# Performance work log

Measured on AMD Instinct MI355X. Metric: run time of the kernel, lower is better.

Reference implementation:

```python
import jax, jax.numpy as jnp
import numpy as np

MAX_LENGTH = 50
EOS_TOKEN = 0
SOS_TOKEN = 1
B, H, V = 64, 1024, 32000


def setup_inputs() -> dict:
    key = jax.random.key(0)
    ks = jax.random.split(key, 11)
    xav = float(np.sqrt(6.0 / (H + H)))  # xavier_uniform over [H,H] slabs
    inv = 1.0 / float(np.sqrt(H))
    return {
        "encoder_output": jax.random.normal(ks[0], (MAX_LENGTH, B, H), jnp.float32),
        "std": jax.random.normal(ks[1], (MAX_LENGTH, B, V), jnp.float32),
        "h": jax.random.normal(ks[2], (B, H), jnp.float32),
        "c": jax.random.normal(ks[3], (B, H), jnp.float32),
        "emb": jax.random.normal(ks[4], (V, H), jnp.float32),
        "w_ih": jax.random.uniform(ks[5], (4, H, H), jnp.float32, -xav, xav),
        "w_hh": jax.random.uniform(ks[6], (4, H, H), jnp.float32, -xav, xav),
        "b_ih": jax.random.normal(ks[7], (4, H), jnp.float32),
        "b_hh": jax.random.normal(ks[8], (4, H), jnp.float32),
        "out_w": jax.random.uniform(ks[9], (H, V), jnp.float32, -inv, inv),
        "out_b": jax.random.uniform(ks[10], (V,), jnp.float32, -inv, inv),
    }


def reference(encoder_output, std, h, c, emb, w_ih, w_hh, b_ih, b_hh, out_w, out_b):
    batch = encoder_output.shape[1]
    tok0 = jnp.full((batch,), SOS_TOKEN, dtype=jnp.int64)

    def step(carry, std_t):
        h, c, tok, active = carry  # active: scalar bool, True while decoding
        x = emb[tok]  # [B,H] embedding gather
        # gates: [4,B,H] = x@W_ih + h@W_hh + biases
        g = (jnp.einsum("bh,ghk->gbk", x, w_ih) + b_ih[:, None, :]
             + jnp.einsum("bh,ghk->gbk", h, w_hh) + b_hh[:, None, :])
        ingate = jax.nn.sigmoid(g[0])
        forgetgate = jax.nn.sigmoid(g[1])
        cellgate = jnp.tanh(g[2])
        outgate = jax.nn.sigmoid(g[3])
        c_new = forgetgate * c + ingate * cellgate
        h_new = outgate * jnp.tanh(c_new)
        logits = h_new @ out_w + out_b + std_t  # [B,V]
        tok_new = jnp.argmax(logits, axis=1).astype(jnp.int64)
        # only commit the step while the decode loop is active
        h2 = jnp.where(active, h_new, h)
        c2 = jnp.where(active, c_new, c)
        tok2 = jnp.where(active, tok_new, tok)
        tok_out = jnp.where(active, tok_new, jnp.zeros_like(tok_new))
        next_active = jnp.logical_and(active, jnp.max(tok_new) > EOS_TOKEN)
        return (h2, c2, tok2, next_active), tok_out

    (h, c, _, _), output_all = jax.lax.scan(
        step, (h, c, tok0, jnp.array(True)), std)
    return output_all, h
```

## Files before the change

kernel.cpp:

```cpp
#include <hip/hip_runtime.h>
#include <cstdint>
#include <cstddef>

#define B 64
#define H 1024
#define V 32000
#define T 50
#define VT 2000
#define GNT 256
#define SW 16.0f
#define SL 2048.0f
#define INV_HI (1.0f/16.0f)
#define INV_LO (1.0f/32768.0f)

typedef _Float16 f16;
typedef _Float16 half8 __attribute__((ext_vector_type(8)));
typedef float f32x4 __attribute__((ext_vector_type(4)));

__device__ __forceinline__ float sigmoidf_(float x) { return 1.0f / (1.0f + expf(-x)); }


__global__ __launch_bounds__(256) void k_packw(const float* __restrict__ out_w,
                                               f16* __restrict__ Whi, f16* __restrict__ Wlo)
{
    const int vt = blockIdx.x >> 3, cg = blockIdx.x & 7;
    const int chunk = cg * 4 + (threadIdx.x >> 6);
    const int q = (threadIdx.x >> 4) & 3, vl = threadIdx.x & 15;
    const int lane = q * 16 + vl;
    half8 h8, l8;
    #pragma unroll
    for (int j = 0; j < 8; ++j) {
        const int k = chunk * 32 + q * 8 + j;
        const float w = out_w[(size_t)k * V + vt * 16 + vl] * SW;
        const f16 hi = (f16)w;
        h8[j] = hi;
        l8[j] = (f16)((w - (float)hi) * SL);
    }
    const size_t pos = ((size_t)(vt * 32 + chunk) * 64 + lane) * 8;
    *(half8*)&Whi[pos] = h8;
    *(half8*)&Wlo[pos] = l8;
}

__global__ __launch_bounds__(256) void k_packg(const float* __restrict__ w_ih,
                                               const float* __restrict__ w_hh,
                                               f16* __restrict__ Ghi, f16* __restrict__ Glo)
{
    const int nt = blockIdx.x >> 4, cg = blockIdx.x & 15;
    const int chunk = cg * 4 + (threadIdx.x >> 6);
    const int q = (threadIdx.x >> 4) & 3, vl = threadIdx.x & 15;
    const int lane = q * 16 + vl;
    const int kk = vl >> 2, g = vl & 3;
    const int kcol = nt * 4 + kk;
    half8 h8, l8;
    #pragma unroll
    for (int j = 0; j < 8; ++j) {
        const int K = chunk * 32 + q * 8 + j;
        const float w = ((K < 1024)
            ? w_ih[(size_t)g * H * H + (size_t)K * H + kcol]
            : w_hh[(size_t)g * H * H + (size_t)(K - 1024) * H + kcol]) * SW;
        const f16 hi = (f16)w;
        h8[j] = hi;
        l8[j] = (f16)((w - (float)hi) * SL);
    }
    const size_t pos = ((size_t)(nt * 64 + chunk) * 64 + lane) * 8;
    *(half8*)&Ghi[pos] = h8;
    *(half8*)&Glo[pos] = l8;
}

__global__ void k_packbias(const float* __restrict__ b_ih, const float* __restrict__ b_hh,
                           float* __restrict__ biasp)
{
    const int n = blockIdx.x * 256 + threadIdx.x;
    const int blk = n >> 4, rem = n & 15, kk = rem >> 2, g = rem & 3;
    const int kcol = blk * 4 + kk;
    biasp[n] = b_ih[g * H + kcol] + b_hh[g * H + kcol];
}

__global__ void k_init(const float* __restrict__ h_in, const float* __restrict__ c_in,
                       const float* __restrict__ emb,
                       float* __restrict__ h_t, float* __restrict__ c_t,
                       f16* __restrict__ Axh, f16* __restrict__ Axl,
                       f16* __restrict__ Ah0h, f16* __restrict__ Ah0l,
                       unsigned long long* __restrict__ keys, int* __restrict__ active,
                       float* __restrict__ out)
{
    if (blockIdx.x == 64) {
        for (int i = threadIdx.x; i < T * B; i += 256) out[i] = 0.0f;
        if (threadIdx.x < B) keys[threadIdx.x] = 0ull;
        if (threadIdx.x == 0) { active[0] = 1; active[1] = 0; }
        return;
    }
    const int b = blockIdx.x, mt = b >> 4;
    #pragma unroll
    for (int i = 0; i < 4; ++i) {
        const int k = threadIdx.x * 4 + i;
        const float hv = h_in[b * H + k];
        const float cv = c_in[b * H + k];
        h_t[k * B + b] = hv;
        c_t[k * B + b] = cv;
        const float xv = emb[H + k];
        const int chunk = k >> 5, lane = ((k >> 3) & 3) * 16 + (b & 15), j = k & 7;
        const size_t pos = ((size_t)(chunk * 4 + mt) * 64 + lane) * 8 + j;
        f16 hi = (f16)hv;
        Ah0h[pos] = hi; Ah0l[pos] = (f16)((hv - (float)hi) * SL);
        hi = (f16)xv;
        Axh[pos] = hi; Axl[pos] = (f16)((xv - (float)hi) * SL);
    }
}

__global__ __launch_bounds__(256) void k_gates(
    const f16* __restrict__ Ghi, const f16* __restrict__ Glo,
    const f16* __restrict__ Axh, const f16* __restrict__ Axl,
    const f16* __restrict__ Ahh, const f16* __restrict__ Ahl,
    f16* __restrict__ Anh, f16* __restrict__ Anl,
    const float* __restrict__ biasp, float* __restrict__ h_t, float* __restrict__ c_t,
    const int* __restrict__ active, int t)
{
    if (!active[t & 1]) return;
    const int tid = threadIdx.x;
    const int s = tid >> 6, lane = tid & 63;
    const int quad = lane >> 4, vl = lane & 15;
    const int nt = blockIdx.x;

    f32x4 acc0[4], acc1[4];
    #pragma unroll
    for (int mt = 0; mt < 4; ++mt) {
        acc0[mt] = (f32x4){0.f, 0.f, 0.f, 0.f};
        acc1[mt] = (f32x4){0.f, 0.f, 0.f, 0.f};
    }

    for (int c = s * 16; c < s * 16 + 16; ++c) {
        const f16* ah = (c < 32) ? Axh : Ahh;
        const f16* al = (c < 32) ? Axl : Ahl;
        const int cc = c & 31;
        const size_t wpos = ((size_t)(nt * 64 + c) * 64 + lane) * 8;
        const half8 whi = *(const half8*)&Ghi[wpos];
        const half8 wlo = *(const half8*)&Glo[wpos];
        #pragma unroll
        for (int mt = 0; mt < 4; ++mt) {
            const size_t apos = ((size_t)(cc * 4 + mt) * 64 + lane) * 8;
            const half8 ahi = *(const half8*)&ah[apos];
            const half8 alo = *(const half8*)&al[apos];
            acc0[mt] = __builtin_amdgcn_mfma_f32_16x16x32_f16(ahi, whi, acc0[mt], 0, 0, 0);
            acc1[mt] = __builtin_amdgcn_mfma_f32_16x16x32_f16(ahi, wlo, acc1[mt], 0, 0, 0);
            acc1[mt] = __builtin_amdgcn_mfma_f32_16x16x32_f16(alo, whi, acc1[mt], 0, 0, 0);
        }
    }

    __shared__ float red[4][64][16];
    __shared__ float gsum[64][17];
    #pragma unroll
    for (int mt = 0; mt < 4; ++mt)
        #pragma unroll
        for (int r = 0; r < 4; ++r)
            red[s][mt * 16 + quad * 4 + r][vl] = acc0[mt][r] * INV_HI + acc1[mt][r] * INV_LO;
    __syncthreads();
    #pragma unroll
    for (int i = 0; i < 4; ++i) {
        const int p = i * 256 + tid;
        const int b = p >> 4, v2 = p & 15;
        gsum[b][v2] = red[0][b][v2] + red[1][b][v2] + red[2][b][v2] + red[3][b][v2]
                    + biasp[nt * 16 + v2];
    }
    __syncthreads();
    {
        const int kk = tid >> 6, b = tid & 63;
        const float ig = sigmoidf_(gsum[b][kk * 4 + 0]);
        const float fg = sigmoidf_(gsum[b][kk * 4 + 1]);
        const float cg = tanhf(gsum[b][kk * 4 + 2]);
        const float og = sigmoidf_(gsum[b][kk * 4 + 3]);
        const int k = nt * 4 + kk;
        const float cv = c_t[k * B + b];
        const float cn = fg * cv + ig * cg;
        const float hn = og * tanhf(cn);
        c_t[k * B + b] = cn;
        h_t[k * B + b] = hn;
        const int chunk = k >> 5, mt = b >> 4, lane2 = ((k >> 3) & 3) * 16 + (b & 15), j = k & 7;
        const size_t pos = ((size_t)(chunk * 4 + mt) * 64 + lane2) * 8 + j;
        const f16 hi = (f16)hn;
        Anh[pos] = hi;
        Anl[pos] = (f16)((hn - (float)hi) * SL);
    }
}

__global__ __launch_bounds__(256) void k_logits(
    const f16* __restrict__ Ahh, const f16* __restrict__ Ahl,
    const f16* __restrict__ Whi, const f16* __restrict__ Wlo,
    const float* __restrict__ out_b, const float* __restrict__ std_,
    unsigned long long* __restrict__ keys, int* __restrict__ active, int t)
{
    const int cur = t & 1;
    if (blockIdx.x == 0 && threadIdx.x == 0) active[cur ^ 1] = 0;
    if (!active[cur]) return;
    const int tid = threadIdx.x;
    const int w = tid >> 6, lane = tid & 63;
    const int quad = lane >> 4, vl = lane & 15;
    const int v0 = blockIdx.x * 64;
    const int vt = blockIdx.x * 4 + w;

    __shared__ float std_s[64][68];
    __shared__ unsigned long long wk[4][64];
    #pragma unroll
    for (int i = 0; i < 4; ++i) {
        const int p = i * 256 + tid;
        const int row = p >> 4, cc = (p & 15) * 4;
        const float4 sv = *(const float4*)&std_[((size_t)t * B + row) * V + v0 + cc];
        *(float4*)&std_s[row][cc] = sv;
    }

    f32x4 acc0[4], acc1[4];
    #pragma unroll
    for (int mt = 0; mt < 4; ++mt) {
        acc0[mt] = (f32x4){0.f, 0.f, 0.f, 0.f};
        acc1[mt] = (f32x4){0.f, 0.f, 0.f, 0.f};
    }
    for (int c = 0; c < 32; ++c) {
        const size_t wpos = ((size_t)(vt * 32 + c) * 64 + lane) * 8;
        const half8 whi = *(const half8*)&Whi[wpos];
        const half8 wlo = *(const half8*)&Wlo[wpos];
        #pragma unroll
        for (int mt = 0; mt < 4; ++mt) {
            const size_t apos = ((size_t)(c * 4 + mt) * 64 + lane) * 8;
            const half8 ahi = *(const half8*)&Ahh[apos];
            const half8 alo = *(const half8*)&Ahl[apos];
            acc0[mt] = __builtin_amdgcn_mfma_f32_16x16x32_f16(ahi, whi, acc0[mt], 0, 0, 0);
            acc1[mt] = __builtin_amdgcn_mfma_f32_16x16x32_f16(ahi, wlo, acc1[mt], 0, 0, 0);
            acc1[mt] = __builtin_amdgcn_mfma_f32_16x16x32_f16(alo, whi, acc1[mt], 0, 0, 0);
        }
    }
    __syncthreads();

    const float outb = out_b[vt * 16 + vl];
    const int v = vt * 16 + vl;
    #pragma unroll
    for (int mt = 0; mt < 4; ++mt) {
        #pragma unroll
        for (int r = 0; r < 4; ++r) {
            const int b = mt * 16 + quad * 4 + r;
            const float val = acc0[mt][r] * INV_HI + acc1[mt][r] * INV_LO
                            + outb + std_s[b][w * 16 + vl];
            const uint32_t fb = __float_as_uint(val);
            const uint32_t mk = (fb & 0x80000000u) ? ~fb : (fb | 0x80000000u);
            unsigned long long key = ((unsigned long long)mk << 32)
                                   | (unsigned)(0x7FFFFFFF - v);
            #pragma unroll
            for (int m = 1; m < 16; m <<= 1) {
                const unsigned long long o = __shfl_xor(key, m, 16);
                if (o > key) key = o;
            }
            if (vl == 0) wk[w][b] = key;
        }
    }
    __syncthreads();
    if (tid < 64) {
        unsigned long long k0 = wk[0][tid];
        const unsigned long long k1 = wk[1][tid], k2 = wk[2][tid], k3 = wk[3][tid];
        if (k1 > k0) k0 = k1;
        if (k2 > k0) k0 = k2;
        if (k3 > k0) k0 = k3;
        atomicMax(&keys[tid], k0);
    }
}

__global__ void k_final(const float* __restrict__ emb,
                        unsigned long long* __restrict__ keys, int* __restrict__ active,
                        float* __restrict__ out,
                        f16* __restrict__ Axh, f16* __restrict__ Axl, int t)
{
    const int cur = t & 1;
    if (!active[cur]) return;
    const int b = blockIdx.x;
    const unsigned long long kk = keys[b];
    const int tokn = 0x7FFFFFFF - (int)(unsigned)(kk & 0xFFFFFFFFull);
    if (threadIdx.x == 0) {
        out[t * B + b] = (float)tokn;
        keys[b] = 0ull;
        if (tokn > 0) atomicOr(&active[cur ^ 1], 1);
    }
    const float* er = emb + (size_t)tokn * H;
    const int mt = b >> 4;
    #pragma unroll
    for (int r = 0; r < 2; ++r) {
        const int k0 = threadIdx.x * 16 + r * 8;
        const float4 x0 = *(const float4*)&er[k0];
        const float4 x1 = *(const float4*)&er[k0 + 4];
        const float xs[8] = {x0.x, x0.y, x0.z, x0.w, x1.x, x1.y, x1.z, x1.w};
        half8 h8, l8;
        #pragma unroll
        for (int j = 0; j < 8; ++j) {
            const f16 hi = (f16)xs[j];
            h8[j] = hi;
            l8[j] = (f16)((xs[j] - (float)hi) * SL);
        }
        const int chunk = k0 >> 5, lane = ((k0 >> 3) & 3) * 16 + (b & 15);
        const size_t pos = ((size_t)(chunk * 4 + mt) * 64 + lane) * 8;
        *(half8*)&Axh[pos] = h8;
        *(half8*)&Axl[pos] = l8;
    }
}

__global__ void k_fin(const float* __restrict__ h_t, float* __restrict__ out)
{
    const int idx = blockIdx.x * 256 + threadIdx.x;
    const int b = idx >> 10, k = idx & 1023;
    out[T * B + idx] = h_t[k * B + b];
}

extern "C" void kernel_launch(void* const* d_in, const int* in_sizes, int n_in,
                              void* d_out, int out_size, void* d_ws, size_t ws_size,
                              hipStream_t stream)
{
    const float* std_  = (const float*)d_in[1];
    const float* h_in  = (const float*)d_in[2];
    const float* c_in  = (const float*)d_in[3];
    const float* emb   = (const float*)d_in[4];
    const float* w_ih  = (const float*)d_in[5];
    const float* w_hh  = (const float*)d_in[6];
    const float* b_ih  = (const float*)d_in[7];
    const float* b_hh  = (const float*)d_in[8];
    const float* out_w = (const float*)d_in[9];
    const float* out_b = (const float*)d_in[10];
    float* out = (float*)d_out;

    f16* Whi = (f16*)d_ws;
    f16* Wlo = Whi + (size_t)H * V;
    f16* Ghi = Wlo + (size_t)H * V;
    f16* Glo = Ghi + (size_t)2048 * 4096;
    f16* Axh = Glo + (size_t)2048 * 4096;
    f16* Axl = Axh + B * H;
    f16* Ah0h = Axl + B * H;
    f16* Ah0l = Ah0h + B * H;
    f16* Ah1h = Ah0l + B * H;
    f16* Ah1l = Ah1h + B * H;
    float* biasp = (float*)(Ah1l + B * H);
    float* h_t = biasp + 4096;
    float* c_t = h_t + B * H;
    unsigned long long* keys = (unsigned long long*)(c_t + B * H);
    int* active = (int*)(keys + B);

    f16* AhH[2] = {Ah0h, Ah1h};
    f16* AhL[2] = {Ah0l, Ah1l};

    k_packw<<<VT * 8, 256, 0, stream>>>(out_w, Whi, Wlo);
    k_packg<<<GNT * 16, 256, 0, stream>>>(w_ih, w_hh, Ghi, Glo);
    k_packbias<<<16, 256, 0, stream>>>(b_ih, b_hh, biasp);
    k_init<<<65, 256, 0, stream>>>(h_in, c_in, emb, h_t, c_t, Axh, Axl,
                                   Ah0h, Ah0l, keys, active, out);
    for (int t = 0; t < T; ++t) {
        const int cur = t & 1, nxt = cur ^ 1;
        k_gates<<<GNT, 256, 0, stream>>>(Ghi, Glo, Axh, Axl, AhH[cur], AhL[cur],
                                         AhH[nxt], AhL[nxt], biasp, h_t, c_t, active, t);
        k_logits<<<V / 64, 256, 0, stream>>>(AhH[nxt], AhL[nxt], Whi, Wlo,
                                             out_b, std_, keys, active, t);
        k_final<<<64, 64, 0, stream>>>(emb, keys, active, out, Axh, Axl, t);
    }
    k_fin<<<256, 256, 0, stream>>>(h_t, out);
}
```

Before: 4.148 ms.

## Fuse final argmax/embedding step into logits kernel via last-block counter

Removes the per-step k_final launch by having the last k_logits block to finish (found with an atomic counter and fences) decode the argmax keys, write tokens, update the active flag and repack the next embedding into the fp16 hi/lo layout. Bias packing is folded into k_init, which removes one more launch. Weight and std loads are marked nontemporal to reduce cache pollution. The saving is about fifty small launches, but the tail work now runs serially inside a single block of 256 threads.

New measurement: 4.953 ms. 19.4% more time.

```diff
diff --git a/kernel.cpp b/kernel.cpp
--- a/kernel.cpp
+++ b/kernel.cpp
@@ -31,7 +31,7 @@
     #pragma unroll
     for (int j = 0; j < 8; ++j) {
         const int k = chunk * 32 + q * 8 + j;
-        const float w = out_w[(size_t)k * V + vt * 16 + vl] * SW;
+        const float w = __builtin_nontemporal_load(&out_w[(size_t)k * V + vt * 16 + vl]) * SW;
         const f16 hi = (f16)w;
         h8[j] = hi;
         l8[j] = (f16)((w - (float)hi) * SL);
@@ -56,8 +56,8 @@
     for (int j = 0; j < 8; ++j) {
         const int K = chunk * 32 + q * 8 + j;
         const float w = ((K < 1024)
-            ? w_ih[(size_t)g * H * H + (size_t)K * H + kcol]
-            : w_hh[(size_t)g * H * H + (size_t)(K - 1024) * H + kcol]) * SW;
+            ? __builtin_nontemporal_load(&w_ih[(size_t)g * H * H + (size_t)K * H + kcol])
+            : __builtin_nontemporal_load(&w_hh[(size_t)g * H * H + (size_t)(K - 1024) * H + kcol])) * SW;
         const f16 hi = (f16)w;
         h8[j] = hi;
         l8[j] = (f16)((w - (float)hi) * SL);
@@ -67,27 +67,27 @@
     *(half8*)&Glo[pos] = l8;
 }
 
-__global__ void k_packbias(const float* __restrict__ b_ih, const float* __restrict__ b_hh,
-                           float* __restrict__ biasp)
-{
-    const int n = blockIdx.x * 256 + threadIdx.x;
-    const int blk = n >> 4, rem = n & 15, kk = rem >> 2, g = rem & 3;
-    const int kcol = blk * 4 + kk;
-    biasp[n] = b_ih[g * H + kcol] + b_hh[g * H + kcol];
-}
-
 __global__ void k_init(const float* __restrict__ h_in, const float* __restrict__ c_in,
                        const float* __restrict__ emb,
+                       const float* __restrict__ b_ih, const float* __restrict__ b_hh,
                        float* __restrict__ h_t, float* __restrict__ c_t,
                        f16* __restrict__ Axh, f16* __restrict__ Axl,
                        f16* __restrict__ Ah0h, f16* __restrict__ Ah0l,
                        unsigned long long* __restrict__ keys, int* __restrict__ active,
-                       float* __restrict__ out)
-{
+                       int* __restrict__ cnt, float* __restrict__ out,
+                       float* __restrict__ biasp)
+{
+    if (blockIdx.x >= 65) {
+        const int n = (blockIdx.x - 65) * 256 + threadIdx.x;
+        const int blk = n >> 4, rem = n & 15, kk = rem >> 2, g = rem & 3;
+        const int kcol = blk * 4 + kk;
+        biasp[n] = b_ih[g * H + kcol] + b_hh[g * H + kcol];
+        return;
+    }
     if (blockIdx.x == 64) {
         for (int i = threadIdx.x; i < T * B; i += 256) out[i] = 0.0f;
         if (threadIdx.x < B) keys[threadIdx.x] = 0ull;
-        if (threadIdx.x == 0) { active[0] = 1; active[1] = 0; }
+        if (threadIdx.x == 0) { active[0] = 1; active[1] = 0; cnt[0] = 0; }
         return;
     }
     const int b = blockIdx.x, mt = b >> 4;
@@ -187,7 +187,10 @@
     const f16* __restrict__ Ahh, const f16* __restrict__ Ahl,
     const f16* __restrict__ Whi, const f16* __restrict__ Wlo,
     const float* __restrict__ out_b, const float* __restrict__ std_,
-    unsigned long long* __restrict__ keys, int* __restrict__ active, int t)
+    const float* __restrict__ emb,
+    unsigned long long* __restrict__ keys, int* __restrict__ active,
+    int* __restrict__ cnt, float* __restrict__ out,
+    f16* __restrict__ Axh, f16* __restrict__ Axl, int t)
 {
     const int cur = t & 1;
     if (blockIdx.x == 0 && threadIdx.x == 0) active[cur ^ 1] = 0;
@@ -204,8 +207,9 @@
     for (int i = 0; i < 4; ++i) {
         const int p = i * 256 + tid;
         const int row = p >> 4, cc = (p & 15) * 4;
-        const float4 sv = *(const float4*)&std_[((size_t)t * B + row) * V + v0 + cc];
-        *(float4*)&std_s[row][cc] = sv;
+        const f32x4 sv = __builtin_nontemporal_load(
+            (const f32x4*)&std_[((size_t)t * B + row) * V + v0 + cc]);
+        *(f32x4*)&std_s[row][cc] = sv;
     }
 
     f32x4 acc0[4], acc1[4];
@@ -260,30 +264,36 @@
         if (k3 > k0) k0 = k3;
         atomicMax(&keys[tid], k0);
     }
-}
-
-__global__ void k_final(const float* __restrict__ emb,
-                        unsigned long long* __restrict__ keys, int* __restrict__ active,
-                        float* __restrict__ out,
-                        f16* __restrict__ Axh, f16* __restrict__ Axl, int t)
-{
-    const int cur = t & 1;
-    if (!active[cur]) return;
-    const int b = blockIdx.x;
-    const unsigned long long kk = keys[b];
-    const int tokn = 0x7FFFFFFF - (int)(unsigned)(kk & 0xFFFFFFFFull);
-    if (threadIdx.x == 0) {
-        out[t * B + b] = (float)tokn;
-        keys[b] = 0ull;
+
+    __shared__ int lastFlag;
+    if (tid == 0) {
+        __threadfence();
+        lastFlag = (atomicAdd(cnt, 1) == (int)gridDim.x - 1);
+    }
+    __syncthreads();
+    if (!lastFlag) return;
+    __threadfence();
+
+    if (tid == 0) cnt[0] = 0;
+    __shared__ int toks[64];
+    if (tid < 64) {
+        const unsigned long long kk = keys[tid];
+        const int tokn = 0x7FFFFFFF - (int)(unsigned)(kk & 0xFFFFFFFFull);
+        toks[tid] = tokn;
+        out[t * B + tid] = (float)tokn;
+        keys[tid] = 0ull;
         if (tokn > 0) atomicOr(&active[cur ^ 1], 1);
     }
+    __syncthreads();
+    const int b = tid >> 2, seg = tid & 3;
+    const int tokn = toks[b];
     const float* er = emb + (size_t)tokn * H;
     const int mt = b >> 4;
-    #pragma unroll
-    for (int r = 0; r < 2; ++r) {
-        const int k0 = threadIdx.x * 16 + r * 8;
-        const float4 x0 = *(const float4*)&er[k0];
-        const float4 x1 = *(const float4*)&er[k0 + 4];
+    #pragma unroll 4
+    for (int i = 0; i < 32; ++i) {
+        const int kk0 = seg * 256 + i * 8;
+        const f32x4 x0 = *(const f32x4*)&er[kk0];
+        const f32x4 x1 = *(const f32x4*)&er[kk0 + 4];
         const float xs[8] = {x0.x, x0.y, x0.z, x0.w, x1.x, x1.y, x1.z, x1.w};
         half8 h8, l8;
         #pragma unroll
@@ -292,8 +302,8 @@
             h8[j] = hi;
             l8[j] = (f16)((xs[j] - (float)hi) * SL);
         }
-        const int chunk = k0 >> 5, lane = ((k0 >> 3) & 3) * 16 + (b & 15);
-        const size_t pos = ((size_t)(chunk * 4 + mt) * 64 + lane) * 8;
+        const int chunk = kk0 >> 5, lane2 = ((kk0 >> 3) & 3) * 16 + (b & 15);
+        const size_t pos = ((size_t)(chunk * 4 + mt) * 64 + lane2) * 8;
         *(half8*)&Axh[pos] = h8;
         *(half8*)&Axl[pos] = l8;
     }
@@ -337,22 +347,22 @@
     float* c_t = h_t + B * H;
     unsigned long long* keys = (unsigned long long*)(c_t + B * H);
     int* active = (int*)(keys + B);
+    int* cnt = active + 2;
 
     f16* AhH[2] = {Ah0h, Ah1h};
     f16* AhL[2] = {Ah0l, Ah1l};
 
     k_packw<<<VT * 8, 256, 0, stream>>>(out_w, Whi, Wlo);
     k_packg<<<GNT * 16, 256, 0, stream>>>(w_ih, w_hh, Ghi, Glo);
-    k_packbias<<<16, 256, 0, stream>>>(b_ih, b_hh, biasp);
-    k_init<<<65, 256, 0, stream>>>(h_in, c_in, emb, h_t, c_t, Axh, Axl,
-                                   Ah0h, Ah0l, keys, active, out);
+    k_init<<<81, 256, 0, stream>>>(h_in, c_in, emb, b_ih, b_hh, h_t, c_t, Axh, Axl,
+                                   Ah0h, Ah0l, keys, active, cnt, out, biasp);
     for (int t = 0; t < T; ++t) {
         const int cur = t & 1, nxt = cur ^ 1;
         k_gates<<<GNT, 256, 0, stream>>>(Ghi, Glo, Axh, Axl, AhH[cur], AhL[cur],
                                          AhH[nxt], AhL[nxt], biasp, h_t, c_t, active, t);
         k_logits<<<V / 64, 256, 0, stream>>>(AhH[nxt], AhL[nxt], Whi, Wlo,
-                                             out_b, std_, keys, active, t);
-        k_final<<<64, 64, 0, stream>>>(emb, keys, active, out, Axh, Axl, t);
+                                             out_b, std_, emb, keys, active, cnt,
+                                             out, Axh, Axl, t);
     }
     k_fin<<<256, 256, 0, stream>>>(h_t, out);
 }
```
